# Optimization experiments

Hardware: AMD Instinct MI355X
Metric: run time of the kernel (lower is better)

Reference implementation:

```python
import jax, jax.numpy as jnp
import numpy as np

N_NODES = 100000
N_EDGES = 1600000
D_IN = 128
D_OUT = 128


def setup_inputs() -> dict:
    key = jax.random.key(0)
    k1, k2, k3 = jax.random.split(key, 3)
    input_matrix = jax.random.normal(k1, (N_NODES, D_IN), dtype=jnp.float32)
    adjacency_coo_matrix = jax.random.randint(k2, (2, N_EDGES), 0, N_NODES, dtype=jnp.int64)
    # xavier-uniform-like init for the projection weights
    limit = float(np.sqrt(6.0 / (D_IN + D_OUT)))
    W = jax.random.uniform(k3, (D_IN, D_OUT), minval=-limit, maxval=limit, dtype=jnp.float32)
    return {"input_matrix": input_matrix, "adjacency_coo_matrix": adjacency_coo_matrix, "W": W}


def reference(input_matrix, adjacency_coo_matrix, W):
    N = input_matrix.shape[0]
    # add self edges (i -> i) for every node
    self_idx = jnp.arange(N, dtype=adjacency_coo_matrix.dtype)
    src = jnp.concatenate([adjacency_coo_matrix[0], self_idx])  # segment ids (rows of output)
    nbr = jnp.concatenate([adjacency_coo_matrix[1], self_idx])  # gather indices
    # gather neighbor features: [E+N, d_in]
    neighbors = input_matrix[nbr]
    # scatter-mean over destination nodes
    summed = jax.ops.segment_sum(neighbors, src, num_segments=N)
    counts = jax.ops.segment_sum(jnp.ones((src.shape[0],), dtype=input_matrix.dtype), src, num_segments=N)
    mean = summed / counts[:, None]  # counts >= 1 thanks to self edges
    # linear projection
    return mean @ W
```

## Files before the change

### kernel.cpp

```cpp
#include <hip/hip_runtime.h>
#include <stdint.h>

#define DIM 128
#define SB 256

typedef unsigned short u16;
typedef unsigned int u32;
typedef __attribute__((ext_vector_type(8))) short short8;
typedef __attribute__((ext_vector_type(4))) float floatx4;
typedef __attribute__((ext_vector_type(4))) float nt_f32x4;
typedef __attribute__((ext_vector_type(4))) int i32x4;

__device__ __forceinline__ u16 f2bf(float f) {
    u32 u = __float_as_uint(f);
    if ((u & 0x7fffffffu) > 0x7f800000u) return (u16)0x7fc0;
    return (u16)((u + 0x7fffu + ((u >> 16) & 1u)) >> 16);
}

__global__ void __launch_bounds__(256) k_wprep(const float* __restrict__ W,
                                               u16* __restrict__ Wbf,
                                               u16* __restrict__ Yzero) {
    int g = blockIdx.x * 256 + threadIdx.x;
    if (g < DIM * DIM) {
        int n = g >> 7, k = g & 127;
        Wbf[g] = f2bf(W[k * DIM + n]);
    }
    if (blockIdx.x == 0 && threadIdx.x < 32)
        ((ushort4*)Yzero)[threadIdx.x] = make_ushort4(0, 0, 0, 0);
}

__global__ void __launch_bounds__(256) k_gemm_y(const float4* __restrict__ X4,
                                                const u16* __restrict__ Wbf,
                                                u16* __restrict__ Ybf,
                                                int* __restrict__ cursor, int N) {
    __shared__ __align__(16) u16 wt[DIM * 136];
    __shared__ __align__(16) u16 a_lds[4][16 * 136];
    int t = threadIdx.x;
    int g = blockIdx.x * 256 + t;
    if (g < N) cursor[g] = 0;
    for (int i = t; i < DIM * 16; i += 256) {
        int row = i >> 4, c8 = i & 15;
        *(short8*)&wt[row * 136 + c8 * 8] = *(const short8*)&Wbf[row * 128 + c8 * 8];
    }
    __syncthreads();
    int w = t >> 6, l = t & 63;
    int q = l >> 4, c = l & 15;
    int row0 = (blockIdx.x * 4 + w) * 16;
    #pragma unroll
    for (int rep = 0; rep < 8; ++rep) {
        int chunk = rep * 64 + l;
        int r = chunk >> 5, c4 = chunk & 31;
        int row = row0 + r;
        float4 v = (row < N) ? X4[(size_t)row * 32 + c4] : make_float4(0.f, 0.f, 0.f, 0.f);
        ushort4 h;
        h.x = f2bf(v.x); h.y = f2bf(v.y); h.z = f2bf(v.z); h.w = f2bf(v.w);
        *(ushort4*)&a_lds[w][r * 136 + c4 * 4] = h;
    }
    __syncthreads();
    floatx4 acc[8] = {};
    #pragma unroll
    for (int kt = 0; kt < 4; ++kt) {
        short8 a = *(const short8*)&a_lds[w][c * 136 + kt * 32 + q * 8];
        #pragma unroll
        for (int nt = 0; nt < 8; ++nt) {
            short8 b = *(const short8*)&wt[(nt * 16 + c) * 136 + kt * 32 + q * 8];
            acc[nt] = __builtin_amdgcn_mfma_f32_16x16x32_bf16(a, b, acc[nt], 0, 0, 0);
        }
    }
    #pragma unroll
    for (int nt = 0; nt < 8; ++nt)
        #pragma unroll
        for (int r = 0; r < 4; ++r)
            a_lds[w][(q * 4 + r) * 136 + nt * 16 + c] = f2bf(acc[nt][r]);
    #pragma unroll
    for (int rep = 0; rep < 8; ++rep) {
        int chunk = rep * 64 + l;
        int r = chunk >> 5, c4 = chunk & 31;
        int row = row0 + r;
        if (row < N)
            ((ushort4*)Ybf)[(size_t)row * 32 + c4] = *(ushort4*)&a_lds[w][r * 136 + c4 * 4];
    }
}

__global__ void __launch_bounds__(256) k_scatter(const int* __restrict__ adj,
                                                 int* __restrict__ cursor,
                                                 int* __restrict__ slots,
                                                 int E, int N, int cap) {
    int r = blockIdx.x & 7;
    int sub = blockIdx.x >> 3;
    int nsub = gridDim.x >> 3;
    int lo = N / 8 * r + min(r, N % 8);
    int hi = lo + N / 8 + (r < N % 8 ? 1 : 0);
    const i32x4* v4 = (const i32x4*)adj;
    int npair = E >> 3;
    for (int p = sub * 256 + threadIdx.x; p < npair; p += nsub * 256) {
        i32x4 s0 = __builtin_nontemporal_load(&v4[2 * p]);
        i32x4 s1 = __builtin_nontemporal_load(&v4[2 * p + 1]);
        int e0 = p * 8;
        int nb[8];
        #pragma unroll
        for (int k = 0; k < 8; ++k)
            nb[k] = __builtin_nontemporal_load(&adj[E + e0 + k]);
        int ds[8] = {s0.x, s0.y, s0.z, s0.w, s1.x, s1.y, s1.z, s1.w};
        #pragma unroll
        for (int k = 0; k < 8; ++k) {
            int d = ds[k];
            if (d < lo || d >= hi) continue;
            int c = atomicAdd(&cursor[d], 1);
            if (c < cap) slots[(size_t)d * cap + c] = ((unsigned)nb[k] < (unsigned)N) ? nb[k] : 0;
        }
    }
    int tail = E & 7;
    if (sub == 0 && threadIdx.x < tail) {
        int e = (E & ~7) + threadIdx.x;
        int d = adj[e];
        if (d >= lo && d < hi) {
            int nbv = adj[E + e];
            int c = atomicAdd(&cursor[d], 1);
            if (c < cap) slots[(size_t)d * cap + c] = ((unsigned)nbv < (unsigned)N) ? nbv : 0;
        }
    }
}

__device__ __forceinline__ void agg_core(const uint4* __restrict__ Yb4,
                                         const int* __restrict__ lst, int deg,
                                         int wid, int grp, int sl, int N,
                                         float4* __restrict__ out4) {
    float acc[8];
    {
        int id0 = (grp == 0) ? wid : N;
        uint4 v = Yb4[(size_t)id0 * 16 + sl];
        u32 c0[4] = {v.x, v.y, v.z, v.w};
        #pragma unroll
        for (int k2 = 0; k2 < 4; ++k2) {
            acc[2 * k2]     = __uint_as_float(c0[k2] << 16);
            acc[2 * k2 + 1] = __uint_as_float(c0[k2] & 0xffff0000u);
        }
    }
    for (int base = 0; base < deg; base += 32) {
        int id[8];
        #pragma unroll
        for (int qi = 0; qi < 8; ++qi) {
            int ee = base + qi * 4 + grp;
            int t = __builtin_nontemporal_load(&lst[ee]);
            id[qi] = (ee < deg) ? t : N;
        }
        uint4 v[8];
        #pragma unroll
        for (int qi = 0; qi < 8; ++qi)
            v[qi] = Yb4[(size_t)id[qi] * 16 + sl];
        #pragma unroll
        for (int qi = 0; qi < 8; ++qi) {
            u32 c0[4] = {v[qi].x, v[qi].y, v[qi].z, v[qi].w};
            #pragma unroll
            for (int k2 = 0; k2 < 4; ++k2) {
                acc[2 * k2]     += __uint_as_float(c0[k2] << 16);
                acc[2 * k2 + 1] += __uint_as_float(c0[k2] & 0xffff0000u);
            }
        }
    }
    #pragma unroll
    for (int j = 0; j < 8; ++j) {
        acc[j] += __shfl_xor(acc[j], 16);
        acc[j] += __shfl_xor(acc[j], 32);
    }
    float inv = 1.0f / (float)(deg + 1);
    if (grp < 2) {
        nt_f32x4 o;
        o.x = acc[grp * 4 + 0] * inv; o.y = acc[grp * 4 + 1] * inv;
        o.z = acc[grp * 4 + 2] * inv; o.w = acc[grp * 4 + 3] * inv;
        __builtin_nontemporal_store(o, (nt_f32x4*)&out4[(size_t)wid * 32 + sl * 2 + grp]);
    }
}

__global__ void __launch_bounds__(256) k_agg_cap(const uint4* __restrict__ Yb4,
                                                 const int* __restrict__ cnt,
                                                 const int* __restrict__ slots,
                                                 float4* __restrict__ out4, int N, int cap) {
    int wid = (blockIdx.x * 256 + threadIdx.x) >> 6;
    int lane = threadIdx.x & 63;
    if (wid >= N) return;
    int deg = min(cnt[wid], cap);
    agg_core(Yb4, slots + (size_t)wid * cap, deg, wid, lane >> 4, lane & 15, N, out4);
}

__global__ void __launch_bounds__(256) k_agg_off(const uint4* __restrict__ Yb4,
                                                 const int* __restrict__ offsets,
                                                 const int* __restrict__ sorted_nbr,
                                                 float4* __restrict__ out4, int N) {
    int wid = (blockIdx.x * 256 + threadIdx.x) >> 6;
    int lane = threadIdx.x & 63;
    if (wid >= N) return;
    int beg = offsets[wid], end = offsets[wid + 1];
    agg_core(Yb4, sorted_nbr + beg, end - beg, wid, lane >> 4, lane & 15, N, out4);
}

__global__ void __launch_bounds__(256) k_hist(const int* __restrict__ adj,
                                              int* __restrict__ counts, int E, int N) {
    int r = blockIdx.x & 7;
    int sub = blockIdx.x >> 3;
    int nsub = gridDim.x >> 3;
    int lo = N / 8 * r + min(r, N % 8);
    int hi = lo + N / 8 + (r < N % 8 ? 1 : 0);
    for (int e = sub * 256 + threadIdx.x; e < E; e += nsub * 256) {
        int d = adj[e];
        if (d >= lo && d < hi) atomicAdd(&counts[d], 1);
    }
}

__global__ void __launch_bounds__(SB) k_bsum(const int* __restrict__ counts,
                                             int* __restrict__ partials, int N) {
    __shared__ int lds[SB];
    int t = threadIdx.x;
    int i = blockIdx.x * SB + t;
    lds[t] = (i < N) ? counts[i] : 0;
    __syncthreads();
    for (int off = SB / 2; off > 0; off >>= 1) {
        if (t < off) lds[t] += lds[t + off];
        __syncthreads();
    }
    if (t == 0) partials[blockIdx.x] = lds[0];
}

__global__ void __launch_bounds__(1024) k_pscan(int* __restrict__ partials,
                                                int* __restrict__ offsets, int nb, int N) {
    __shared__ int lds[1024];
    int t = threadIdx.x;
    int v0 = (t < nb) ? partials[t] : 0;
    lds[t] = v0;
    __syncthreads();
    for (int off = 1; off < 1024; off <<= 1) {
        int v = (t >= off) ? lds[t - off] : 0;
        __syncthreads();
        lds[t] += v;
        __syncthreads();
    }
    if (t < nb) partials[t] = lds[t] - v0;
    if (t == 1023) offsets[N] = lds[1023];
}

__global__ void __launch_bounds__(SB) k_scan_final(const int* __restrict__ counts_in,
                                                   const int* __restrict__ partials,
                                                   int* __restrict__ offsets,
                                                   int* __restrict__ cursor, int N) {
    __shared__ int lds[SB];
    int t = threadIdx.x;
    int i = blockIdx.x * SB + t;
    int c = (i < N) ? counts_in[i] : 0;
    lds[t] = c;
    __syncthreads();
    for (int off = 1; off < SB; off <<= 1) {
        int v = (t >= off) ? lds[t - off] : 0;
        __syncthreads();
        lds[t] += v;
        __syncthreads();
    }
    int excl = lds[t] - c + partials[blockIdx.x];
    if (i < N) {
        offsets[i] = excl;
        cursor[i] = excl;
    }
}

__global__ void __launch_bounds__(256) k_reorder(const int* __restrict__ adj,
                                                 int* __restrict__ cursor,
                                                 int* __restrict__ sorted_nbr, int E, int N) {
    int r = blockIdx.x & 7;
    int sub = blockIdx.x >> 3;
    int nsub = gridDim.x >> 3;
    int lo = N / 8 * r + min(r, N % 8);
    int hi = lo + N / 8 + (r < N % 8 ? 1 : 0);
    for (int e = sub * 256 + threadIdx.x; e < E; e += nsub * 256) {
        int d = adj[e];
        if (d < lo || d >= hi) continue;
        int nb = adj[E + e];
        int pos = atomicAdd(&cursor[d], 1);
        sorted_nbr[pos] = ((unsigned)nb < (unsigned)N) ? nb : 0;
    }
}

extern "C" void kernel_launch(void* const* d_in, const int* in_sizes, int n_in,
                              void* d_out, int out_size, void* d_ws, size_t ws_size,
                              hipStream_t stream) {
    int N = in_sizes[0] / DIM;
    int E = in_sizes[1] / 2;
    const float* X = (const float*)d_in[0];
    const int* adj = (const int*)d_in[1];
    const float* W = (const float*)d_in[2];
    float* out = (float*)d_out;

    int gemm_blocks = (N + 63) / 64;
    size_t cur_b  = (size_t)N * 4;
    size_t y_b    = ((size_t)N + 1) * DIM * 2;
    size_t wbf_b  = (size_t)DIM * DIM * 2;

    int cap = 0;
    if (ws_size >= cur_b + (size_t)N * 64 * 4 + y_b + wbf_b) cap = 64;
    else if (ws_size >= cur_b + (size_t)N * 48 * 4 + y_b + wbf_b) cap = 48;

    if (cap) {
        int* cursor = (int*)d_ws;
        int* slots  = cursor + N;
        u16* Ybf    = (u16*)(slots + (size_t)N * cap);
        u16* Wbf    = Ybf + ((size_t)N + 1) * DIM;

        k_wprep<<<64, 256, 0, stream>>>(W, Wbf, Ybf + (size_t)N * DIM);
        k_gemm_y<<<gemm_blocks, 256, 0, stream>>>((const float4*)X, Wbf, Ybf, cursor, N);
        k_scatter<<<2048, 256, 0, stream>>>(adj, cursor, slots, E, N, cap);
        k_agg_cap<<<(N + 3) / 4, 256, 0, stream>>>((const uint4*)Ybf, cursor, slots,
                                                   (float4*)out, N, cap);
    } else {
        int nb = (N + SB - 1) / SB;
        int* cursor     = (int*)d_ws;
        int* offsets    = cursor + N;
        int* sorted_nbr = offsets + (N + 1);
        int* partials   = sorted_nbr + E;
        u16* Ybf        = (u16*)(partials + 512);
        u16* Wbf        = Ybf + ((size_t)N + 1) * DIM;

        k_wprep<<<64, 256, 0, stream>>>(W, Wbf, Ybf + (size_t)N * DIM);
        k_gemm_y<<<gemm_blocks, 256, 0, stream>>>((const float4*)X, Wbf, Ybf, cursor, N);
        k_hist<<<1024, 256, 0, stream>>>(adj, cursor, E, N);
        k_bsum<<<nb, SB, 0, stream>>>(cursor, partials, N);
        k_pscan<<<1, 1024, 0, stream>>>(partials, offsets, nb, N);
        k_scan_final<<<nb, SB, 0, stream>>>(cursor, partials, offsets, cursor, N);
        k_reorder<<<1024, 256, 0, stream>>>(adj, cursor, sorted_nbr, E, N);
        k_agg_off<<<(N + 3) / 4, 256, 0, stream>>>((const uint4*)Ybf, offsets, sorted_nbr,
                                                   (float4*)out, N);
    }
}
```

Measured before the change: 258.6 us.

## Pad per-node atomic cursors and batch atomics in scatter kernel

Spaces each node's cursor counter out by up to 32 ints (128 bytes), depending on available workspace, so concurrent atomicAdds from different nodes no longer share cache lines. The scatter loop now issues all eight atomics before doing the slot stores, which lets their latencies overlap. It also drops the nontemporal loads of the adjacency array. In exchange, the cursor array grows by up to 32x, adding memory footprint and scattered zeroing writes in the GEMM kernel.

```diff
diff --git a/kernel.cpp b/kernel.cpp
--- a/kernel.cpp
+++ b/kernel.cpp
@@ -9,7 +9,6 @@
 typedef __attribute__((ext_vector_type(8))) short short8;
 typedef __attribute__((ext_vector_type(4))) float floatx4;
 typedef __attribute__((ext_vector_type(4))) float nt_f32x4;
-typedef __attribute__((ext_vector_type(4))) int i32x4;
 
 __device__ __forceinline__ u16 f2bf(float f) {
     u32 u = __float_as_uint(f);
@@ -32,12 +31,12 @@
 __global__ void __launch_bounds__(256) k_gemm_y(const float4* __restrict__ X4,
                                                 const u16* __restrict__ Wbf,
                                                 u16* __restrict__ Ybf,
-                                                int* __restrict__ cursor, int N) {
+                                                int* __restrict__ cursor, int N, int psh) {
     __shared__ __align__(16) u16 wt[DIM * 136];
     __shared__ __align__(16) u16 a_lds[4][16 * 136];
     int t = threadIdx.x;
     int g = blockIdx.x * 256 + t;
-    if (g < N) cursor[g] = 0;
+    if (g < N) cursor[(size_t)g << psh] = 0;
     for (int i = t; i < DIM * 16; i += 256) {
         int row = i >> 4, c8 = i & 15;
         *(short8*)&wt[row * 136 + c8 * 8] = *(const short8*)&Wbf[row * 128 + c8 * 8];
@@ -85,29 +84,33 @@
 __global__ void __launch_bounds__(256) k_scatter(const int* __restrict__ adj,
                                                  int* __restrict__ cursor,
                                                  int* __restrict__ slots,
-                                                 int E, int N, int cap) {
+                                                 int E, int N, int cap, int psh) {
     int r = blockIdx.x & 7;
     int sub = blockIdx.x >> 3;
     int nsub = gridDim.x >> 3;
     int lo = N / 8 * r + min(r, N % 8);
     int hi = lo + N / 8 + (r < N % 8 ? 1 : 0);
-    const i32x4* v4 = (const i32x4*)adj;
+    const int4* v4 = (const int4*)adj;
     int npair = E >> 3;
     for (int p = sub * 256 + threadIdx.x; p < npair; p += nsub * 256) {
-        i32x4 s0 = __builtin_nontemporal_load(&v4[2 * p]);
-        i32x4 s1 = __builtin_nontemporal_load(&v4[2 * p + 1]);
+        int4 s0 = v4[2 * p];
+        int4 s1 = v4[2 * p + 1];
         int e0 = p * 8;
         int nb[8];
         #pragma unroll
-        for (int k = 0; k < 8; ++k)
-            nb[k] = __builtin_nontemporal_load(&adj[E + e0 + k]);
+        for (int k = 0; k < 8; ++k) nb[k] = adj[E + e0 + k];
         int ds[8] = {s0.x, s0.y, s0.z, s0.w, s1.x, s1.y, s1.z, s1.w};
+        int cc[8];
         #pragma unroll
         for (int k = 0; k < 8; ++k) {
-            int d = ds[k];
-            if (d < lo || d >= hi) continue;
-            int c = atomicAdd(&cursor[d], 1);
-            if (c < cap) slots[(size_t)d * cap + c] = ((unsigned)nb[k] < (unsigned)N) ? nb[k] : 0;
+            bool hit = (ds[k] >= lo) & (ds[k] < hi);
+            cc[k] = hit ? atomicAdd(&cursor[(size_t)ds[k] << psh], 1) : cap;
+        }
+        #pragma unroll
+        for (int k = 0; k < 8; ++k) {
+            if (cc[k] < cap)
+                slots[(size_t)ds[k] * cap + cc[k]] =
+                    ((unsigned)nb[k] < (unsigned)N) ? nb[k] : 0;
         }
     }
     int tail = E & 7;
@@ -116,7 +119,7 @@
         int d = adj[e];
         if (d >= lo && d < hi) {
             int nbv = adj[E + e];
-            int c = atomicAdd(&cursor[d], 1);
+            int c = atomicAdd(&cursor[(size_t)d << psh], 1);
             if (c < cap) slots[(size_t)d * cap + c] = ((unsigned)nbv < (unsigned)N) ? nbv : 0;
         }
     }
@@ -176,11 +179,12 @@
 __global__ void __launch_bounds__(256) k_agg_cap(const uint4* __restrict__ Yb4,
                                                  const int* __restrict__ cnt,
                                                  const int* __restrict__ slots,
-                                                 float4* __restrict__ out4, int N, int cap) {
+                                                 float4* __restrict__ out4, int N,
+                                                 int cap, int psh) {
     int wid = (blockIdx.x * 256 + threadIdx.x) >> 6;
     int lane = threadIdx.x & 63;
     if (wid >= N) return;
-    int deg = min(cnt[wid], cap);
+    int deg = min(cnt[(size_t)wid << psh], cap);
     agg_core(Yb4, slots + (size_t)wid * cap, deg, wid, lane >> 4, lane & 15, N, out4);
 }
 
@@ -290,25 +294,32 @@
     float* out = (float*)d_out;
 
     int gemm_blocks = (N + 63) / 64;
-    size_t cur_b  = (size_t)N * 4;
     size_t y_b    = ((size_t)N + 1) * DIM * 2;
     size_t wbf_b  = (size_t)DIM * DIM * 2;
 
-    int cap = 0;
-    if (ws_size >= cur_b + (size_t)N * 64 * 4 + y_b + wbf_b) cap = 64;
-    else if (ws_size >= cur_b + (size_t)N * 48 * 4 + y_b + wbf_b) cap = 48;
+    int cap = 0, psh = 0;
+    {
+        const int pshs[5] = {5, 4, 3, 2, 0};
+        for (int i = 0; i < 5 && !cap; ++i) {
+            size_t cur_b = ((size_t)N << pshs[i]) * 4;
+            if (ws_size >= cur_b + (size_t)N * 64 * 4 + y_b + wbf_b) { cap = 64; psh = pshs[i]; }
+        }
+        if (!cap && ws_size >= (size_t)N * 4 + (size_t)N * 48 * 4 + y_b + wbf_b) {
+            cap = 48; psh = 0;
+        }
+    }
 
     if (cap) {
         int* cursor = (int*)d_ws;
-        int* slots  = cursor + N;
+        int* slots  = cursor + ((size_t)N << psh);
         u16* Ybf    = (u16*)(slots + (size_t)N * cap);
         u16* Wbf    = Ybf + ((size_t)N + 1) * DIM;
 
         k_wprep<<<64, 256, 0, stream>>>(W, Wbf, Ybf + (size_t)N * DIM);
-        k_gemm_y<<<gemm_blocks, 256, 0, stream>>>((const float4*)X, Wbf, Ybf, cursor, N);
-        k_scatter<<<2048, 256, 0, stream>>>(adj, cursor, slots, E, N, cap);
+        k_gemm_y<<<gemm_blocks, 256, 0, stream>>>((const float4*)X, Wbf, Ybf, cursor, N, psh);
+        k_scatter<<<2048, 256, 0, stream>>>(adj, cursor, slots, E, N, cap, psh);
         k_agg_cap<<<(N + 3) / 4, 256, 0, stream>>>((const uint4*)Ybf, cursor, slots,
-                                                   (float4*)out, N, cap);
+                                                   (float4*)out, N, cap, psh);
     } else {
         int nb = (N + SB - 1) / SB;
         int* cursor     = (int*)d_ws;
@@ -319,7 +330,7 @@
         u16* Wbf        = Ybf + ((size_t)N + 1) * DIM;
 
         k_wprep<<<64, 256, 0, stream>>>(W, Wbf, Ybf + (size_t)N * DIM);
-        k_gemm_y<<<gemm_blocks, 256, 0, stream>>>((const float4*)X, Wbf, Ybf, cursor, N);
+        k_gemm_y<<<gemm_blocks, 256, 0, stream>>>((const float4*)X, Wbf, Ybf, cursor, N, 0);
         k_hist<<<1024, 256, 0, stream>>>(adj, cursor, E, N);
         k_bsum<<<nb, SB, 0, stream>>>(cursor, partials, N);
         k_pscan<<<1, 1024, 0, stream>>>(partials, offsets, nb, N);
```

Result: no change. 259.6 us (+0.4%).

## Load GEMM A operand directly into registers, batch scatter atomics, enlarge GEMM blocks

Applied to the files above, without the earlier changes.

The projection GEMM kernel now reads X straight from global memory into the MFMA operand layout and writes bf16 results directly, with no LDS staging tile or extra barrier. Blocks grow to 512 threads so each W tile loaded into LDS serves 8 waves instead of 4. The scatter kernel issues all 8 atomics before any slot stores so they can overlap, and it uses plain loads instead of nontemporal ones. The direct global reads and 2-byte scattered stores are less coalesced than the old staged copies, which may offset the savings.

```diff
diff --git a/kernel.cpp b/kernel.cpp
--- a/kernel.cpp
+++ b/kernel.cpp
@@ -9,7 +9,6 @@
 typedef __attribute__((ext_vector_type(8))) short short8;
 typedef __attribute__((ext_vector_type(4))) float floatx4;
 typedef __attribute__((ext_vector_type(4))) float nt_f32x4;
-typedef __attribute__((ext_vector_type(4))) int i32x4;
 
 __device__ __forceinline__ u16 f2bf(float f) {
     u32 u = __float_as_uint(f);
@@ -29,38 +28,38 @@
         ((ushort4*)Yzero)[threadIdx.x] = make_ushort4(0, 0, 0, 0);
 }
 
-__global__ void __launch_bounds__(256) k_gemm_y(const float4* __restrict__ X4,
+__global__ void __launch_bounds__(512) k_gemm_y(const float4* __restrict__ X4,
                                                 const u16* __restrict__ Wbf,
                                                 u16* __restrict__ Ybf,
                                                 int* __restrict__ cursor, int N) {
     __shared__ __align__(16) u16 wt[DIM * 136];
-    __shared__ __align__(16) u16 a_lds[4][16 * 136];
     int t = threadIdx.x;
-    int g = blockIdx.x * 256 + t;
+    int g = blockIdx.x * 512 + t;
     if (g < N) cursor[g] = 0;
-    for (int i = t; i < DIM * 16; i += 256) {
+    for (int i = t; i < DIM * 16; i += 512) {
         int row = i >> 4, c8 = i & 15;
         *(short8*)&wt[row * 136 + c8 * 8] = *(const short8*)&Wbf[row * 128 + c8 * 8];
     }
     __syncthreads();
     int w = t >> 6, l = t & 63;
     int q = l >> 4, c = l & 15;
-    int row0 = (blockIdx.x * 4 + w) * 16;
+    int row0 = (blockIdx.x * 8 + w) * 16;
+    size_t mr = (size_t)min(row0 + c, N - 1) * 32;
+    float4 u[8];
     #pragma unroll
-    for (int rep = 0; rep < 8; ++rep) {
-        int chunk = rep * 64 + l;
-        int r = chunk >> 5, c4 = chunk & 31;
-        int row = row0 + r;
-        float4 v = (row < N) ? X4[(size_t)row * 32 + c4] : make_float4(0.f, 0.f, 0.f, 0.f);
-        ushort4 h;
-        h.x = f2bf(v.x); h.y = f2bf(v.y); h.z = f2bf(v.z); h.w = f2bf(v.w);
-        *(ushort4*)&a_lds[w][r * 136 + c4 * 4] = h;
-    }
-    __syncthreads();
+    for (int kt = 0; kt < 4; ++kt) {
+        u[2 * kt]     = X4[mr + kt * 8 + q * 2];
+        u[2 * kt + 1] = X4[mr + kt * 8 + q * 2 + 1];
+    }
     floatx4 acc[8] = {};
     #pragma unroll
     for (int kt = 0; kt < 4; ++kt) {
-        short8 a = *(const short8*)&a_lds[w][c * 136 + kt * 32 + q * 8];
+        short8 a;
+        float4 u0 = u[2 * kt], u1 = u[2 * kt + 1];
+        a[0] = (short)f2bf(u0.x); a[1] = (short)f2bf(u0.y);
+        a[2] = (short)f2bf(u0.z); a[3] = (short)f2bf(u0.w);
+        a[4] = (short)f2bf(u1.x); a[5] = (short)f2bf(u1.y);
+        a[6] = (short)f2bf(u1.z); a[7] = (short)f2bf(u1.w);
         #pragma unroll
         for (int nt = 0; nt < 8; ++nt) {
             short8 b = *(const short8*)&wt[(nt * 16 + c) * 136 + kt * 32 + q * 8];
@@ -68,17 +67,14 @@
         }
     }
     #pragma unroll
-    for (int nt = 0; nt < 8; ++nt)
-        #pragma unroll
-        for (int r = 0; r < 4; ++r)
-            a_lds[w][(q * 4 + r) * 136 + nt * 16 + c] = f2bf(acc[nt][r]);
-    #pragma unroll
-    for (int rep = 0; rep < 8; ++rep) {
-        int chunk = rep * 64 + l;
-        int r = chunk >> 5, c4 = chunk & 31;
-        int row = row0 + r;
-        if (row < N)
-            ((ushort4*)Ybf)[(size_t)row * 32 + c4] = *(ushort4*)&a_lds[w][r * 136 + c4 * 4];
+    for (int r = 0; r < 4; ++r) {
+        int orow = row0 + q * 4 + r;
+        if (orow < N) {
+            u16* yrow = Ybf + (size_t)orow * DIM;
+            #pragma unroll
+            for (int nt = 0; nt < 8; ++nt)
+                yrow[nt * 16 + c] = f2bf(acc[nt][r]);
+        }
     }
 }
 
@@ -91,23 +87,27 @@
     int nsub = gridDim.x >> 3;
     int lo = N / 8 * r + min(r, N % 8);
     int hi = lo + N / 8 + (r < N % 8 ? 1 : 0);
-    const i32x4* v4 = (const i32x4*)adj;
+    const int4* v4 = (const int4*)adj;
     int npair = E >> 3;
     for (int p = sub * 256 + threadIdx.x; p < npair; p += nsub * 256) {
-        i32x4 s0 = __builtin_nontemporal_load(&v4[2 * p]);
-        i32x4 s1 = __builtin_nontemporal_load(&v4[2 * p + 1]);
+        int4 s0 = v4[2 * p];
+        int4 s1 = v4[2 * p + 1];
         int e0 = p * 8;
         int nb[8];
         #pragma unroll
-        for (int k = 0; k < 8; ++k)
-            nb[k] = __builtin_nontemporal_load(&adj[E + e0 + k]);
+        for (int k = 0; k < 8; ++k) nb[k] = adj[E + e0 + k];
         int ds[8] = {s0.x, s0.y, s0.z, s0.w, s1.x, s1.y, s1.z, s1.w};
+        int cc[8];
         #pragma unroll
         for (int k = 0; k < 8; ++k) {
-            int d = ds[k];
-            if (d < lo || d >= hi) continue;
-            int c = atomicAdd(&cursor[d], 1);
-            if (c < cap) slots[(size_t)d * cap + c] = ((unsigned)nb[k] < (unsigned)N) ? nb[k] : 0;
+            bool hit = (ds[k] >= lo) & (ds[k] < hi);
+            cc[k] = hit ? atomicAdd(&cursor[ds[k]], 1) : cap;
+        }
+        #pragma unroll
+        for (int k = 0; k < 8; ++k) {
+            if (cc[k] < cap)
+                slots[(size_t)ds[k] * cap + cc[k]] =
+                    ((unsigned)nb[k] < (unsigned)N) ? nb[k] : 0;
         }
     }
     int tail = E & 7;
@@ -289,7 +289,7 @@
     const float* W = (const float*)d_in[2];
     float* out = (float*)d_out;
 
-    int gemm_blocks = (N + 63) / 64;
+    int gemm_blocks = (N + 127) / 128;
     size_t cur_b  = (size_t)N * 4;
     size_t y_b    = ((size_t)N + 1) * DIM * 2;
     size_t wbf_b  = (size_t)DIM * DIM * 2;
@@ -305,7 +305,7 @@
         u16* Wbf    = Ybf + ((size_t)N + 1) * DIM;
 
         k_wprep<<<64, 256, 0, stream>>>(W, Wbf, Ybf + (size_t)N * DIM);
-        k_gemm_y<<<gemm_blocks, 256, 0, stream>>>((const float4*)X, Wbf, Ybf, cursor, N);
+        k_gemm_y<<<gemm_blocks, 512, 0, stream>>>((const float4*)X, Wbf, Ybf, cursor, N);
         k_scatter<<<2048, 256, 0, stream>>>(adj, cursor, slots, E, N, cap);
         k_agg_cap<<<(N + 3) / 4, 256, 0, stream>>>((const uint4*)Ybf, cursor, slots,
                                                    (float4*)out, N, cap);
@@ -319,7 +319,7 @@
         u16* Wbf        = Ybf + ((size_t)N + 1) * DIM;
 
         k_wprep<<<64, 256, 0, stream>>>(W, Wbf, Ybf + (size_t)N * DIM);
-        k_gemm_y<<<gemm_blocks, 256, 0, stream>>>((const float4*)X, Wbf, Ybf, cursor, N);
+        k_gemm_y<<<gemm_blocks, 512, 0, stream>>>((const float4*)X, Wbf, Ybf, cursor, N);
         k_hist<<<1024, 256, 0, stream>>>(adj, cursor, E, N);
         k_bsum<<<nb, SB, 0, stream>>>(cursor, partials, N);
         k_pscan<<<1, 1024, 0, stream>>>(partials, offsets, nb, N);
```

Measured after the change: 246.5 us. 1.05x faster.
